# Performance work log

Measured on AMD Instinct MI355X. Metric: run time of the kernel, lower is better.

Reference implementation:

```python
import jax, jax.numpy as jnp
import numpy as np
from jax import lax

B, P, T = 64, 16, 256
I, H, O = 256, 512, 5
V = 50000


def setup_inputs() -> dict:
    key = jax.random.key(0)
    ks = jax.random.split(key, 16)
    xav = lambda k, shape: jax.random.normal(k, shape, dtype=jnp.float32) * np.sqrt(2.0 / (shape[-2] + shape[-1]))
    inp = {
        "x": jax.random.randint(ks[0], (B, P, T), 0, V),
        "emb": jax.random.normal(ks[1], (V, I), dtype=jnp.float32) * 0.02,
        "W_forget_x": xav(ks[2], (P, I, H)),
        "W_forget_h": xav(ks[3], (H, H)),
        "b_forget": jnp.zeros((H,), jnp.float32),
        "W_ic_x": xav(ks[4], (P, I, H)),
        "W_ic_h": xav(ks[5], (H, H)),
        "b_ic": jnp.zeros((H,), jnp.float32),
        "W_in_x": xav(ks[6], (P, I, H)),
        "W_in_h": xav(ks[7], (H, H)),
        "b_in": jnp.zeros((H,), jnp.float32),
        "W_o_x": xav(ks[8], (P, I, H)),
        "W_o_h": xav(ks[9], (H, H)),
        "b_o": jnp.zeros((H,), jnp.float32),
        "W_lin": xav(ks[10], (H, O)),
        "b_lin": jnp.zeros((O,), jnp.float32),
    }
    return inp


def reference(x, emb, W_forget_x, W_forget_h, b_forget, W_ic_x, W_ic_h, b_ic,
              W_in_x, W_in_h, b_in, W_o_x, W_o_h, b_o, W_lin, b_lin):
    # padding_idx=0: row 0 of the embedding table is zero
    tbl = emb.at[0].set(0.0)
    xe = tbl[x]  # [B, P, T, I]
    # x-side gate pre-activations, summed over POS tags, hoisted out of the recurrence
    pre_f = jnp.einsum('bpti,pih->tbh', xe, W_forget_x) + b_forget  # [T, B, H]
    pre_i = jnp.einsum('bpti,pih->tbh', xe, W_ic_x) + b_ic
    pre_g = jnp.einsum('bpti,pih->tbh', xe, W_in_x) + b_in
    pre_o = jnp.einsum('bpti,pih->tbh', xe, W_o_x) + b_o

    def step(carry, pres):
        h, c = carry
        pf, pi, pg, po = pres
        f = jax.nn.sigmoid(pf + h @ W_forget_h)
        i = jax.nn.sigmoid(pi + h @ W_ic_h)
        g = jnp.tanh(pg + h @ W_in_h)
        o = jax.nn.sigmoid(po + h @ W_o_h)
        c = f * c + i * g
        h = o * jnp.tanh(c)
        return (h, c), None

    bs = x.shape[0]
    h0 = jnp.zeros((bs, W_forget_h.shape[0]), jnp.float32)
    c0 = jnp.zeros_like(h0)
    (h_t, c_t), _ = lax.scan(step, (h0, c0), (pre_f, pre_i, pre_g, pre_o))
    out = h_t @ W_lin + b_lin  # [B, O]
    return out, h_t, c_t
```

## Files before the change

### kernel.cpp

```cpp
#include <hip/hip_runtime.h>
#include <stdint.h>

#define DEVI __device__ __forceinline__

typedef __bf16 bf16x8 __attribute__((ext_vector_type(8)));
typedef float floatx4 __attribute__((ext_vector_type(4)));

DEVI uint16_t f2bf(float f) {
  union { float f; uint32_t u; } c; c.f = f;
  uint32_t u = c.u;
  return (uint16_t)((u + 0x7fffu + ((u >> 16) & 1u)) >> 16);
}
DEVI float bf2f(uint16_t h) {
  union { uint32_t u; float f; } c; c.u = ((uint32_t)h) << 16;
  return c.f;
}
DEVI void load_lds_16(const void* g, void* l) {
  __builtin_amdgcn_global_load_lds(
      (const __attribute__((address_space(1))) void*)g,
      (__attribute__((address_space(3))) void*)l, 16, 0, 0);
}
DEVI float sigm(float x) { return 1.f / (1.f + __expf(-x)); }
DEVI float tanh_s(float x) {
  float xc = fminf(fmaxf(x, -15.f), 15.f);
  float e = __expf(2.f * xc);
  return (e - 1.f) / (e + 1.f);
}

static constexpr size_t OFF_EMB   = 0;
static constexpr size_t OFF_HBUF  = 0;
static constexpr size_t OFF_WXT   = 25600000;
static constexpr size_t OFF_WHT   = OFF_WXT + 16777216;
static constexpr size_t OFF_BIAS  = OFF_WHT + 2097152;
static constexpr size_t OFF_PRE   = OFF_BIAS + 8192;
static constexpr size_t OFF_FLAGS = OFF_PRE + 67108864;
static constexpr size_t OFF_HF    = OFF_FLAGS + 4096;
static constexpr size_t OFF_CF    = OFF_HF + 131072;

__global__ __launch_bounds__(256) void k_emb_cvt(const float* __restrict__ emb,
                                                 uint16_t* __restrict__ dst) {
  size_t tid = (size_t)blockIdx.x * 256 + threadIdx.x;
  size_t e = tid * 8;
  int v = (int)(e >> 8);
  const float4* s = (const float4*)(emb + e);
  float4 f0 = s[0], f1 = s[1];
  if (v == 0) { f0 = make_float4(0.f, 0.f, 0.f, 0.f); f1 = f0; }
  uint32_t w0 = f2bf(f0.x) | ((uint32_t)f2bf(f0.y) << 16);
  uint32_t w1 = f2bf(f0.z) | ((uint32_t)f2bf(f0.w) << 16);
  uint32_t w2 = f2bf(f1.x) | ((uint32_t)f2bf(f1.y) << 16);
  uint32_t w3 = f2bf(f1.z) | ((uint32_t)f2bf(f1.w) << 16);
  *(uint4*)(dst + e) = make_uint4(w0, w1, w2, w3);
}

__global__ __launch_bounds__(256) void k_wt(const float* __restrict__ w0, const float* __restrict__ w1,
                                            const float* __restrict__ w2, const float* __restrict__ w3,
                                            int K, uint16_t* __restrict__ dst) {
  __shared__ float tile[64 * 64];
  int k0 = blockIdx.x * 64;
  int n0 = blockIdx.y * 64;
  int h0 = blockIdx.y * 16;
  int g = threadIdx.x >> 6, di = threadIdx.x & 63;
  const float* w = (g == 0) ? w0 : (g == 1) ? w1 : (g == 2) ? w2 : w3;
  const float4* src = (const float4*)(w + (size_t)(k0 + di) * 512 + h0);
  float4 a = src[0], b = src[1], c = src[2], d = src[3];
  float vals[16] = {a.x, a.y, a.z, a.w, b.x, b.y, b.z, b.w,
                    c.x, c.y, c.z, c.w, d.x, d.y, d.z, d.w};
#pragma unroll
  for (int dh = 0; dh < 16; ++dh) tile[(dh * 4 + g) * 64 + di] = vals[dh];
  __syncthreads();
  int nl = threadIdx.x >> 2, ch = threadIdx.x & 3;
  uint32_t wb[8];
#pragma unroll
  for (int j = 0; j < 8; ++j) {
    float lo = tile[nl * 64 + ch * 16 + j * 2];
    float hi = tile[nl * 64 + ch * 16 + j * 2 + 1];
    wb[j] = f2bf(lo) | ((uint32_t)f2bf(hi) << 16);
  }
  uint4* dp = (uint4*)(dst + (size_t)(n0 + nl) * K + k0 + ch * 16);
  dp[0] = make_uint4(wb[0], wb[1], wb[2], wb[3]);
  dp[1] = make_uint4(wb[4], wb[5], wb[6], wb[7]);
}

__global__ __launch_bounds__(256) void k_bias(const float* __restrict__ b0, const float* __restrict__ b1,
                                              const float* __restrict__ b2, const float* __restrict__ b3,
                                              float* __restrict__ dst) {
  int n = blockIdx.x * 256 + threadIdx.x;
  int h = n >> 2, g = n & 3;
  const float* b = (g == 0) ? b0 : (g == 1) ? b1 : (g == 2) ? b2 : b3;
  dst[n] = b[h];
}

__global__ __launch_bounds__(256) void k_gemm(const uint16_t* __restrict__ embbf,
                                              const int* __restrict__ x,
                                              const uint16_t* __restrict__ wxt,
                                              uint16_t* __restrict__ pre) {
  __shared__ uint16_t As[128 * 64];
  __shared__ uint16_t Bs[128 * 64];
  const int tid = threadIdx.x;
  const int wv = tid >> 6, ln = tid & 63;
  const int wm = wv >> 1, wn = wv & 1;
  const int M0 = blockIdx.x * 128, N0 = blockIdx.y * 128;
  const int srow = ln >> 3, schunk = ln & 7;

  const int* xrow[4];
  const uint16_t* bbase[4];
  uint16_t* ldsA[4];
  uint16_t* ldsB[4];
#pragma unroll
  for (int j = 0; j < 4; ++j) {
    int r = j * 32 + wv * 8 + srow;
    int m = M0 + r;
    int t = m >> 6, b = m & 63;
    xrow[j] = x + b * 4096 + t;
    bbase[j] = wxt + (size_t)(N0 + r) * 4096 + schunk * 8;
    ldsA[j] = As + (j * 32 + wv * 8) * 64;
    ldsB[j] = Bs + (j * 32 + wv * 8) * 64;
  }

  const int q = ln >> 4, l16 = ln & 15;
  int aoff[4], boff[4];
#pragma unroll
  for (int mt = 0; mt < 4; ++mt) aoff[mt] = (wm * 64 + mt * 16 + l16) * 64 + q * 8;
#pragma unroll
  for (int nt = 0; nt < 4; ++nt) boff[nt] = (wn * 64 + nt * 16 + l16) * 64 + q * 8;

  floatx4 acc[4][4] = {};

  for (int p = 0; p < 16; ++p) {
    const uint16_t* abase[4];
#pragma unroll
    for (int j = 0; j < 4; ++j) {
      int idx = xrow[j][p << 8];
      abase[j] = embbf + (size_t)idx * 256 + schunk * 8;
    }
#pragma unroll 1
    for (int ki = 0; ki < 4; ++ki) {
      __syncthreads();
#pragma unroll
      for (int j = 0; j < 4; ++j) load_lds_16(abase[j] + ki * 64, ldsA[j]);
#pragma unroll
      for (int j = 0; j < 4; ++j) load_lds_16(bbase[j] + p * 256 + ki * 64, ldsB[j]);
      __syncthreads();
#pragma unroll
      for (int kk = 0; kk < 2; ++kk) {
        bf16x8 a[4];
#pragma unroll
        for (int mt = 0; mt < 4; ++mt) a[mt] = *(const bf16x8*)(As + aoff[mt] + kk * 32);
#pragma unroll
        for (int nt = 0; nt < 4; ++nt) {
          bf16x8 bv = *(const bf16x8*)(Bs + boff[nt] + kk * 32);
#pragma unroll
          for (int mt = 0; mt < 4; ++mt)
            acc[mt][nt] = __builtin_amdgcn_mfma_f32_16x16x32_bf16(a[mt], bv, acc[mt][nt], 0, 0, 0);
        }
      }
    }
  }

#pragma unroll
  for (int mt = 0; mt < 4; ++mt) {
    int mg = M0 + wm * 64 + mt * 16 + q * 4;
#pragma unroll
    for (int nt = 0; nt < 4; ++nt) {
      int ng = N0 + wn * 64 + nt * 16 + l16;
#pragma unroll
      for (int r = 0; r < 4; ++r)
        pre[(size_t)(mg + r) * 2048 + ng] = f2bf(acc[mt][nt][r]);
    }
  }
}

__global__ __launch_bounds__(256) void k_rec(const uint16_t* __restrict__ pre,
                                             const uint16_t* __restrict__ wht,
                                             const float* __restrict__ bias,
                                             uint16_t* __restrict__ hbufs,
                                             int* __restrict__ flags,
                                             float* __restrict__ hfin,
                                             float* __restrict__ cfin) {
  __shared__ uint16_t Ahs[16 * 544];
  __shared__ uint16_t pres[2][16 * 128];
  __shared__ float gates[16 * 128];

  const int tid = threadIdx.x;
  const int wv = tid >> 6, ln = tid & 63;
  const int q = ln >> 4, l16 = ln & 15;
  const int bg = blockIdx.x >> 4, cg = blockIdx.x & 15;
  const int N0 = cg * 128;

  bf16x8 Bfrag[16][2];
#pragma unroll
  for (int kc = 0; kc < 16; ++kc)
#pragma unroll
    for (int nt = 0; nt < 2; ++nt) {
      int n = N0 + wv * 32 + nt * 16 + l16;
      Bfrag[kc][nt] = *(const bf16x8*)(wht + (size_t)n * 512 + kc * 32 + q * 8);
    }
  float breg[2];
#pragma unroll
  for (int nt = 0; nt < 2; ++nt) breg[nt] = bias[N0 + wv * 32 + nt * 16 + l16];

  float creg[2] = {0.f, 0.f};

  {
    const uint16_t* g = pre + (size_t)(bg * 16 + wv * 4 + (ln >> 4)) * 2048 + N0 + (ln & 15) * 8;
    load_lds_16(g, (uint16_t*)pres[0] + wv * 512);
  }

  for (int t = 0; t < 256; ++t) {
    if (t > 0 && ln < 16) {
      int v;
      do {
        v = __hip_atomic_load(&flags[bg * 16 + ln], __ATOMIC_RELAXED, __HIP_MEMORY_SCOPE_AGENT);
      } while (v < t);
    }

    if (t == 0) {
#pragma unroll
      for (int j = 0; j < 4; ++j) {
        int r = wv * 4 + j;
        *(uint4*)(Ahs + r * 544 + ln * 8) = make_uint4(0, 0, 0, 0);
      }
    } else {
      const uint16_t* hsrc = hbufs + (size_t)(t - 1) * 32768 + (size_t)bg * 16 * 512;
#pragma unroll
      for (int j = 0; j < 4; ++j) {
        int r = wv * 4 + j;
        load_lds_16(hsrc + r * 512 + ln * 8, Ahs + r * 544);
      }
    }
    {
      int tn = (t < 255) ? t + 1 : 255;
      const uint16_t* g = pre + (size_t)(tn * 64 + bg * 16 + wv * 4 + (ln >> 4)) * 2048 + N0 + (ln & 15) * 8;
      load_lds_16(g, (uint16_t*)pres[(t + 1) & 1] + wv * 512);
    }
    __syncthreads();

    floatx4 acc[2] = {};
#pragma unroll
    for (int kc = 0; kc < 16; ++kc) {
      bf16x8 a = *(const bf16x8*)(Ahs + l16 * 544 + kc * 32 + q * 8);
#pragma unroll
      for (int nt = 0; nt < 2; ++nt)
        acc[nt] = __builtin_amdgcn_mfma_f32_16x16x32_bf16(a, Bfrag[kc][nt], acc[nt], 0, 0, 0);
    }

    const uint16_t* pcur = (const uint16_t*)pres[t & 1];
#pragma unroll
    for (int nt = 0; nt < 2; ++nt) {
      int n_l = wv * 32 + nt * 16 + l16;
#pragma unroll
      for (int r = 0; r < 4; ++r) {
        int row = q * 4 + r;
        gates[row * 128 + n_l] = acc[nt][r] + breg[nt] + bf2f(pcur[row * 128 + n_l]);
      }
    }
    __syncthreads();

    {
      uint16_t* hdst = hbufs + (size_t)t * 32768;
      int item = tid * 2;
      int b_l = item >> 5, h_l = item & 31;
      float4 v0 = *(const float4*)(gates + b_l * 128 + h_l * 4);
      float4 v1 = *(const float4*)(gates + b_l * 128 + h_l * 4 + 4);
      float f0 = sigm(v0.x), i0 = sigm(v0.y), g0 = tanh_s(v0.z), o0 = sigm(v0.w);
      float f1 = sigm(v1.x), i1 = sigm(v1.y), g1 = tanh_s(v1.z), o1 = sigm(v1.w);
      float c0 = f0 * creg[0] + i0 * g0; creg[0] = c0;
      float c1 = f1 * creg[1] + i1 * g1; creg[1] = c1;
      float h0 = o0 * tanh_s(c0), h1 = o1 * tanh_s(c1);
      uint32_t pk = (uint32_t)f2bf(h0) | ((uint32_t)f2bf(h1) << 16);
      size_t idx = (size_t)(bg * 16 + b_l) * 512 + (size_t)cg * 32 + h_l;
      __hip_atomic_store((uint32_t*)(hdst + idx), pk, __ATOMIC_RELAXED, __HIP_MEMORY_SCOPE_AGENT);
      if (t == 255) {
        hfin[idx] = h0; hfin[idx + 1] = h1;
        cfin[idx] = c0; cfin[idx + 1] = c1;
      }
    }
    __syncthreads();
    if (tid == 0)
      __hip_atomic_store(&flags[bg * 16 + cg], t + 1, __ATOMIC_RELAXED, __HIP_MEMORY_SCOPE_AGENT);
  }
}

__global__ __launch_bounds__(256) void k_final(const float* __restrict__ h, const float* __restrict__ c,
                                               const float* __restrict__ wl, const float* __restrict__ bl,
                                               float* __restrict__ out) {
  __shared__ float red[256];
  int b = blockIdx.x, t = threadIdx.x;
  const float* hb = h + (size_t)b * 512;
  if (t < 128) {
    ((float4*)(out + 320 + (size_t)b * 512))[t] = ((const float4*)hb)[t];
    ((float4*)(out + 320 + 32768 + (size_t)b * 512))[t] = ((const float4*)(c + (size_t)b * 512))[t];
  }
  float h0 = hb[t], h1 = hb[t + 256];
  for (int o = 0; o < 5; ++o) {
    red[t] = h0 * wl[t * 5 + o] + h1 * wl[(t + 256) * 5 + o];
    __syncthreads();
    for (int s = 128; s > 0; s >>= 1) {
      if (t < s) red[t] += red[t + s];
      __syncthreads();
    }
    if (t == 0) out[b * 5 + o] = red[0] + bl[o];
    __syncthreads();
  }
}

extern "C" void kernel_launch(void* const* d_in, const int* in_sizes, int n_in,
                              void* d_out, int out_size, void* d_ws, size_t ws_size,
                              hipStream_t stream) {
  const int*   x   = (const int*)d_in[0];
  const float* emb = (const float*)d_in[1];
  const float* wfx = (const float*)d_in[2];
  const float* wfh = (const float*)d_in[3];
  const float* bf_ = (const float*)d_in[4];
  const float* wix = (const float*)d_in[5];
  const float* wih = (const float*)d_in[6];
  const float* bi_ = (const float*)d_in[7];
  const float* wgx = (const float*)d_in[8];
  const float* wgh = (const float*)d_in[9];
  const float* bg_ = (const float*)d_in[10];
  const float* wox = (const float*)d_in[11];
  const float* woh = (const float*)d_in[12];
  const float* bo_ = (const float*)d_in[13];
  const float* wl  = (const float*)d_in[14];
  const float* bl  = (const float*)d_in[15];
  float* out = (float*)d_out;
  char* ws = (char*)d_ws;

  uint16_t* embbf = (uint16_t*)(ws + OFF_EMB);
  uint16_t* hbufs = (uint16_t*)(ws + OFF_HBUF);
  uint16_t* wxt   = (uint16_t*)(ws + OFF_WXT);
  uint16_t* wht   = (uint16_t*)(ws + OFF_WHT);
  float*    bias  = (float*)(ws + OFF_BIAS);
  uint16_t* pre   = (uint16_t*)(ws + OFF_PRE);
  int*      flags = (int*)(ws + OFF_FLAGS);
  float*    hfin  = (float*)(ws + OFF_HF);
  float*    cfin  = (float*)(ws + OFF_CF);

  hipLaunchKernelGGL(k_emb_cvt, dim3(6250), dim3(256), 0, stream, emb, embbf);
  hipLaunchKernelGGL(k_wt, dim3(64, 32), dim3(256), 0, stream, wfx, wix, wgx, wox, 4096, wxt);
  hipLaunchKernelGGL(k_wt, dim3(8, 32), dim3(256), 0, stream, wfh, wih, wgh, woh, 512, wht);
  hipLaunchKernelGGL(k_bias, dim3(8), dim3(256), 0, stream, bf_, bi_, bg_, bo_, bias);
  hipLaunchKernelGGL(k_gemm, dim3(128, 16), dim3(256), 0, stream, embbf, x, wxt, pre);
  hipLaunchKernelGGL(k_rec, dim3(64), dim3(256), 0, stream, pre, wht, bias, hbufs, flags, hfin, cfin);
  hipLaunchKernelGGL(k_final, dim3(64), dim3(256), 0, stream, hfin, cfin, wl, bl, out);
}
```

Measured before the change: 1.180 ms.

## Replace flag-based inter-block sync with timestamp-tagged h exchange in consumed pre buffer

The recurrent kernel no longer publishes h and then a separate per-block flag behind two barriers. Each thread now stores a 64-bit word that holds the bf16 h pair in the low half and the step number in the high half. Consumers spin directly on those tagged words, so data and readiness arrive together. The exchange buffers for steps two and later reuse pre-activation rows that are already consumed, and LDS h is double-buffered, letting the kernel drop two __syncthreads per step. It also splits the MFMA accumulation into two chains and pads the gates tile. The cost is that every consumer thread polls 16 words instead of one flag, and reusing the pre buffer depends on a subtle ordering of the prefetch reads.

```diff
diff --git a/kernel.cpp b/kernel.cpp
--- a/kernel.cpp
+++ b/kernel.cpp
@@ -2,6 +2,7 @@
 #include <stdint.h>
 
 #define DEVI __device__ __forceinline__
+typedef unsigned long long ull;
 
 typedef __bf16 bf16x8 __attribute__((ext_vector_type(8)));
 typedef float floatx4 __attribute__((ext_vector_type(4)));
@@ -28,13 +29,12 @@
 }
 
 static constexpr size_t OFF_EMB   = 0;
-static constexpr size_t OFF_HBUF  = 0;
+static constexpr size_t OFF_TS01  = 0;
 static constexpr size_t OFF_WXT   = 25600000;
 static constexpr size_t OFF_WHT   = OFF_WXT + 16777216;
 static constexpr size_t OFF_BIAS  = OFF_WHT + 2097152;
 static constexpr size_t OFF_PRE   = OFF_BIAS + 8192;
-static constexpr size_t OFF_FLAGS = OFF_PRE + 67108864;
-static constexpr size_t OFF_HF    = OFF_FLAGS + 4096;
+static constexpr size_t OFF_HF    = OFF_PRE + 67108864 + 4096;
 static constexpr size_t OFF_CF    = OFF_HF + 131072;
 
 __global__ __launch_bounds__(256) void k_emb_cvt(const float* __restrict__ emb,
@@ -170,16 +170,16 @@
   }
 }
 
-__global__ __launch_bounds__(256) void k_rec(const uint16_t* __restrict__ pre,
+__global__ __launch_bounds__(256) void k_rec(const uint16_t* pre,
+                                             char* preb,
+                                             char* scratch,
                                              const uint16_t* __restrict__ wht,
                                              const float* __restrict__ bias,
-                                             uint16_t* __restrict__ hbufs,
-                                             int* __restrict__ flags,
                                              float* __restrict__ hfin,
                                              float* __restrict__ cfin) {
-  __shared__ uint16_t Ahs[16 * 544];
+  __shared__ uint16_t Ahs[2][16 * 544];
   __shared__ uint16_t pres[2][16 * 128];
-  __shared__ float gates[16 * 128];
+  __shared__ float gates[16 * 132];
 
   const int tid = threadIdx.x;
   const int wv = tid >> 6, ln = tid & 63;
@@ -199,85 +199,99 @@
 #pragma unroll
   for (int nt = 0; nt < 2; ++nt) breg[nt] = bias[N0 + wv * 32 + nt * 16 + l16];
 
+  const int prow = wv * 4 + (ln >> 4);
+  const int pj = ln & 15;
+  const int erow = ln >> 2;
+  const int es = ln & 3;
   float creg[2] = {0.f, 0.f};
 
+  for (int i = tid; i < 4352; i += 256) ((uint32_t*)Ahs[0])[i] = 0;
   {
     const uint16_t* g = pre + (size_t)(bg * 16 + wv * 4 + (ln >> 4)) * 2048 + N0 + (ln & 15) * 8;
     load_lds_16(g, (uint16_t*)pres[0] + wv * 512);
   }
 
   for (int t = 0; t < 256; ++t) {
-    if (t > 0 && ln < 16) {
-      int v;
-      do {
-        v = __hip_atomic_load(&flags[bg * 16 + ln], __ATOMIC_RELAXED, __HIP_MEMORY_SCOPE_AGENT);
-      } while (v < t);
-    }
-
-    if (t == 0) {
-#pragma unroll
-      for (int j = 0; j < 4; ++j) {
-        int r = wv * 4 + j;
-        *(uint4*)(Ahs + r * 544 + ln * 8) = make_uint4(0, 0, 0, 0);
+    if (t > 0) {
+      const char* sb = (t - 1 < 2) ? scratch + (size_t)(t - 1) * 262144
+                                   : preb + (size_t)(t - 3) * 262144;
+      const ull* pp = (const ull*)(sb + (size_t)bg * 65536 + prow * 2048 + pj * 8);
+      const uint32_t want = (uint32_t)t;
+      ull v[16];
+      bool ok = false;
+      while (!ok) {
+        ok = true;
+#pragma unroll
+        for (int j = 0; j < 16; ++j)
+          v[j] = __hip_atomic_load(pp + j * 16, __ATOMIC_RELAXED, __HIP_MEMORY_SCOPE_AGENT);
+#pragma unroll
+        for (int j = 0; j < 16; ++j)
+          ok = ok && ((uint32_t)(v[j] >> 32) == want);
+        if (!ok) __builtin_amdgcn_s_sleep(1);
       }
-    } else {
-      const uint16_t* hsrc = hbufs + (size_t)(t - 1) * 32768 + (size_t)bg * 16 * 512;
-#pragma unroll
-      for (int j = 0; j < 4; ++j) {
-        int r = wv * 4 + j;
-        load_lds_16(hsrc + r * 512 + ln * 8, Ahs + r * 544);
-      }
-    }
-    {
-      int tn = (t < 255) ? t + 1 : 255;
-      const uint16_t* g = pre + (size_t)(tn * 64 + bg * 16 + wv * 4 + (ln >> 4)) * 2048 + N0 + (ln & 15) * 8;
-      load_lds_16(g, (uint16_t*)pres[(t + 1) & 1] + wv * 512);
+      uint16_t* dr = Ahs[t & 1] + prow * 544;
+#pragma unroll
+      for (int j = 0; j < 16; ++j)
+        *(uint32_t*)(dr + 2 * pj + 32 * j) = (uint32_t)v[j];
     }
     __syncthreads();
 
-    floatx4 acc[2] = {};
-#pragma unroll
-    for (int kc = 0; kc < 16; ++kc) {
-      bf16x8 a = *(const bf16x8*)(Ahs + l16 * 544 + kc * 32 + q * 8);
+    const uint16_t* Ab = Ahs[t & 1];
+    floatx4 a0[2] = {}, a1[2] = {};
+#pragma unroll
+    for (int kc = 0; kc < 8; ++kc) {
+      bf16x8 a = *(const bf16x8*)(Ab + l16 * 544 + kc * 32 + q * 8);
 #pragma unroll
       for (int nt = 0; nt < 2; ++nt)
-        acc[nt] = __builtin_amdgcn_mfma_f32_16x16x32_bf16(a, Bfrag[kc][nt], acc[nt], 0, 0, 0);
+        a0[nt] = __builtin_amdgcn_mfma_f32_16x16x32_bf16(a, Bfrag[kc][nt], a0[nt], 0, 0, 0);
+    }
+#pragma unroll
+    for (int kc = 8; kc < 16; ++kc) {
+      bf16x8 a = *(const bf16x8*)(Ab + l16 * 544 + kc * 32 + q * 8);
+#pragma unroll
+      for (int nt = 0; nt < 2; ++nt)
+        a1[nt] = __builtin_amdgcn_mfma_f32_16x16x32_bf16(a, Bfrag[kc][nt], a1[nt], 0, 0, 0);
     }
 
     const uint16_t* pcur = (const uint16_t*)pres[t & 1];
 #pragma unroll
     for (int nt = 0; nt < 2; ++nt) {
       int n_l = wv * 32 + nt * 16 + l16;
+      floatx4 s = a0[nt] + a1[nt];
 #pragma unroll
       for (int r = 0; r < 4; ++r) {
         int row = q * 4 + r;
-        gates[row * 128 + n_l] = acc[nt][r] + breg[nt] + bf2f(pcur[row * 128 + n_l]);
+        gates[row * 132 + n_l] = s[r] + breg[nt] + bf2f(pcur[row * 128 + n_l]);
       }
     }
-    __syncthreads();
 
     {
-      uint16_t* hdst = hbufs + (size_t)t * 32768;
-      int item = tid * 2;
-      int b_l = item >> 5, h_l = item & 31;
-      float4 v0 = *(const float4*)(gates + b_l * 128 + h_l * 4);
-      float4 v1 = *(const float4*)(gates + b_l * 128 + h_l * 4 + 4);
+      float4 v0 = *(const float4*)(gates + erow * 132 + wv * 32 + es * 8);
+      float4 v1 = *(const float4*)(gates + erow * 132 + wv * 32 + es * 8 + 4);
       float f0 = sigm(v0.x), i0 = sigm(v0.y), g0 = tanh_s(v0.z), o0 = sigm(v0.w);
       float f1 = sigm(v1.x), i1 = sigm(v1.y), g1 = tanh_s(v1.z), o1 = sigm(v1.w);
       float c0 = f0 * creg[0] + i0 * g0; creg[0] = c0;
       float c1 = f1 * creg[1] + i1 * g1; creg[1] = c1;
       float h0 = o0 * tanh_s(c0), h1 = o1 * tanh_s(c1);
-      uint32_t pk = (uint32_t)f2bf(h0) | ((uint32_t)f2bf(h1) << 16);
-      size_t idx = (size_t)(bg * 16 + b_l) * 512 + (size_t)cg * 32 + h_l;
-      __hip_atomic_store((uint32_t*)(hdst + idx), pk, __ATOMIC_RELAXED, __HIP_MEMORY_SCOPE_AGENT);
+      char* sbw = (t < 2) ? scratch + (size_t)t * 262144
+                          : preb + (size_t)(t - 2) * 262144;
+      int pair = cg * 16 + wv * 4 + es;
+      ull pk = (ull)((uint32_t)f2bf(h0) | ((uint32_t)f2bf(h1) << 16)) |
+               ((ull)(uint32_t)(t + 1) << 32);
+      __hip_atomic_store((ull*)(sbw + (size_t)bg * 65536 + erow * 2048 + pair * 8),
+                         pk, __ATOMIC_RELAXED, __HIP_MEMORY_SCOPE_AGENT);
       if (t == 255) {
+        size_t idx = (size_t)(bg * 16 + erow) * 512 + cg * 32 + wv * 8 + es * 2;
         hfin[idx] = h0; hfin[idx + 1] = h1;
         cfin[idx] = c0; cfin[idx + 1] = c1;
       }
     }
-    __syncthreads();
-    if (tid == 0)
-      __hip_atomic_store(&flags[bg * 16 + cg], t + 1, __ATOMIC_RELAXED, __HIP_MEMORY_SCOPE_AGENT);
+
+    {
+      int tn = (t < 255) ? t + 1 : 255;
+      const uint16_t* g = pre + (size_t)(tn * 64 + bg * 16 + wv * 4 + (ln >> 4)) * 2048 + N0 + (ln & 15) * 8;
+      load_lds_16(g, (uint16_t*)pres[(t + 1) & 1] + wv * 512);
+    }
   }
 }
 
@@ -327,12 +341,10 @@
   char* ws = (char*)d_ws;
 
   uint16_t* embbf = (uint16_t*)(ws + OFF_EMB);
-  uint16_t* hbufs = (uint16_t*)(ws + OFF_HBUF);
   uint16_t* wxt   = (uint16_t*)(ws + OFF_WXT);
   uint16_t* wht   = (uint16_t*)(ws + OFF_WHT);
   float*    bias  = (float*)(ws + OFF_BIAS);
   uint16_t* pre   = (uint16_t*)(ws + OFF_PRE);
-  int*      flags = (int*)(ws + OFF_FLAGS);
   float*    hfin  = (float*)(ws + OFF_HF);
   float*    cfin  = (float*)(ws + OFF_CF);
 
@@ -341,6 +353,7 @@
   hipLaunchKernelGGL(k_wt, dim3(8, 32), dim3(256), 0, stream, wfh, wih, wgh, woh, 512, wht);
   hipLaunchKernelGGL(k_bias, dim3(8), dim3(256), 0, stream, bf_, bi_, bg_, bo_, bias);
   hipLaunchKernelGGL(k_gemm, dim3(128, 16), dim3(256), 0, stream, embbf, x, wxt, pre);
-  hipLaunchKernelGGL(k_rec, dim3(64), dim3(256), 0, stream, pre, wht, bias, hbufs, flags, hfin, cfin);
+  hipLaunchKernelGGL(k_rec, dim3(64), dim3(256), 0, stream, pre, (char*)(ws + OFF_PRE),
+                     ws + OFF_TS01, wht, bias, hfin, cfin);
   hipLaunchKernelGGL(k_final, dim3(64), dim3(256), 0, stream, hfin, cfin, wl, bl, out);
 }
```

Measured after the change: 1.142 ms. 3.2% less time.
